# Kernel tuning notes

Measured on AMD Instinct MI355X. Metric: run time of the kernel, lower is better.

Reference implementation:

```python
import jax, jax.numpy as jnp
import numpy as np

C = 256
NUM_HEADS = 4
GROUPS = 8
EPS = 1e-5


def setup_inputs() -> dict:
    key = jax.random.key(0)
    ks = jax.random.split(key, 7)
    B, H, W = 4, 64, 64
    x = jax.random.normal(ks[0], (B, C, H, W), dtype=jnp.float32)
    # GroupNorm affine params
    norm_w = jnp.ones((C,), dtype=jnp.float32)
    norm_b = jnp.zeros((C,), dtype=jnp.float32)
    # 1x1 convs == channel-mixing matrices
    qkv_w = jax.random.normal(ks[1], (3 * C, C), dtype=jnp.float32) * (C ** -0.5)
    qkv_b = jnp.zeros((3 * C,), dtype=jnp.float32)
    proj_w = jax.random.normal(ks[2], (C, C), dtype=jnp.float32) * (C ** -0.5)
    proj_b = jnp.zeros((C,), dtype=jnp.float32)
    return {"x": x, "norm_w": norm_w, "norm_b": norm_b,
            "qkv_w": qkv_w, "qkv_b": qkv_b,
            "proj_w": proj_w, "proj_b": proj_b}


def _group_norm(x, w, b):
    B, Cc, H, W = x.shape
    xr = x.reshape(B, GROUPS, Cc // GROUPS, H * W)
    mean = xr.mean(axis=(2, 3), keepdims=True)
    var = xr.var(axis=(2, 3), keepdims=True)
    xn = ((xr - mean) * jax.lax.rsqrt(var + EPS)).reshape(B, Cc, H, W)
    return xn * w[None, :, None, None] + b[None, :, None, None]


def reference(x, norm_w, norm_b, qkv_w, qkv_b, proj_w, proj_b):
    B, Cc, H, W = x.shape
    nh = NUM_HEADS
    d = Cc // nh
    h = _group_norm(x, norm_w, norm_b)
    # 1x1 conv: channel matmul
    qkv = jnp.einsum('oc,bchw->bohw', qkv_w, h) + qkv_b[None, :, None, None]
    q, k, v = jnp.split(qkv, 3, axis=1)
    q = q.reshape(B, nh, d, H * W)
    k = k.reshape(B, nh, d, H * W)
    v = v.reshape(B, nh, d, H * W)
    scale = d ** -0.5
    attn = jnp.einsum('bhci,bhcj->bhij', q, k) * scale  # [B, nh, HW, HW]
    attn = jax.nn.softmax(attn, axis=-1)
    o = jnp.einsum('bhij,bhcj->bhci', attn, v).reshape(B, Cc, H, W)
    out = jnp.einsum('oc,bchw->bohw', proj_w, o) + proj_b[None, :, None, None]
    return x + out
```

## Files before the change

kernel.cpp:

```cpp
#include <hip/hip_runtime.h>

typedef unsigned short u16;
typedef __attribute__((ext_vector_type(8))) short bf16x8;
typedef __attribute__((ext_vector_type(4))) float f32x4;
typedef __attribute__((ext_vector_type(16))) float f32x16;
typedef __attribute__((ext_vector_type(2))) int i32x2;

#define MFMA16(A, B, C) __builtin_amdgcn_mfma_f32_16x16x32_bf16((A), (B), (C), 0, 0, 0)
#define MFMA32(A, B, C) __builtin_amdgcn_mfma_f32_32x32x16_bf16((A), (B), (C), 0, 0, 0)

#define BB 4
#define CC 256
#define HW 4096
#define NH 4
#define HD 64

#define QSCALE 0.18033688f

__device__ __forceinline__ u16 f2bf(float f) {
  unsigned int u = __builtin_bit_cast(unsigned int, f);
  u += 0x7fffu + ((u >> 16) & 1u);
  return (u16)(u >> 16);
}

__device__ __forceinline__ unsigned cvtpk(float a, float b) {
  unsigned r;
  asm("v_cvt_pk_bf16_f32 %0, %1, %2" : "=v"(r) : "v"(a), "v"(b));
  return r;
}

__global__ __launch_bounds__(256) void w2bf_kernel(const float* __restrict__ qw,
                                                   const float* __restrict__ pw,
                                                   u16* __restrict__ wbf) {
  int idx = (blockIdx.x * 256 + threadIdx.x) * 4;
  const int NQ = 768 * 256;
  const float* src = (idx < NQ) ? (qw + idx) : (pw + (idx - NQ));
  float4 v = *(const float4*)src;
  union { u16 u[4]; uint2 w; } pk;
  pk.u[0] = f2bf(v.x); pk.u[1] = f2bf(v.y);
  pk.u[2] = f2bf(v.z); pk.u[3] = f2bf(v.w);
  *(uint2*)(wbf + idx) = pk.w;
}

__global__ __launch_bounds__(256) void gn_partial_kernel(const float* __restrict__ x,
                                                         float* __restrict__ partial) {
  const float4* p = (const float4*)(x + (size_t)blockIdx.x * 16384);
  float s = 0.f, ss = 0.f;
  for (int i = threadIdx.x; i < 4096; i += 256) {
    float4 v = p[i];
    s += (v.x + v.y) + (v.z + v.w);
    ss += (v.x * v.x + v.y * v.y) + (v.z * v.z + v.w * v.w);
  }
#pragma unroll
  for (int msk = 32; msk; msk >>= 1) {
    s += __shfl_xor(s, msk);
    ss += __shfl_xor(ss, msk);
  }
  __shared__ float red[2][4];
  int wave = threadIdx.x >> 6;
  if ((threadIdx.x & 63) == 0) { red[0][wave] = s; red[1][wave] = ss; }
  __syncthreads();
  if (threadIdx.x == 0) {
    partial[blockIdx.x] = red[0][0] + red[0][1] + red[0][2] + red[0][3];
    partial[256 + blockIdx.x] = red[1][0] + red[1][1] + red[1][2] + red[1][3];
  }
}

__global__ __launch_bounds__(64) void gn_final_kernel(const float* __restrict__ partial,
                                                      float* __restrict__ stats) {
  int bg = threadIdx.x;
  if (bg < 32) {
    float S = 0.f, SS = 0.f;
#pragma unroll
    for (int sp = 0; sp < 8; ++sp) {
      S += partial[bg * 8 + sp];
      SS += partial[256 + bg * 8 + sp];
    }
    const float invN = 1.0f / 131072.0f;
    float mean = S * invN;
    float var = SS * invN - mean * mean;
    stats[bg] = mean;
    stats[32 + bg] = rsqrtf(var + 1e-5f);
  }
}

__global__ __launch_bounds__(256) void norm_t_kernel(const float* __restrict__ x,
                                                     const float* __restrict__ nw,
                                                     const float* __restrict__ nb,
                                                     const float* __restrict__ stats,
                                                     u16* __restrict__ h_t) {
  int b = blockIdx.y;
  int s = blockIdx.x * 64 + (threadIdx.x & 63);
  int w = threadIdx.x >> 6;
  const float* xb = x + (size_t)b * CC * HW;
  u16* hb = h_t + ((size_t)b * HW + s) * CC;
#pragma unroll
  for (int cc = 0; cc < 8; ++cc) {
    int c0 = w * 64 + cc * 8;
    union { u16 u[8]; uint4 v; } pk;
#pragma unroll
    for (int j = 0; j < 8; ++j) {
      int c = c0 + j;
      int g = c >> 5;
      float mean = stats[b * 8 + g];
      float rstd = stats[32 + b * 8 + g];
      float a = nw[c] * rstd;
      float bb2 = nb[c] - mean * a;
      float vv = xb[(size_t)c * HW + s];
      pk.u[j] = f2bf(vv * a + bb2);
    }
    *(uint4*)(hb + c0) = pk.v;
  }
}

__global__ __launch_bounds__(256) void gemm_qk_kernel(const u16* __restrict__ h_t,
                                                      const u16* __restrict__ wbf,
                                                      const float* __restrict__ qb,
                                                      u16* __restrict__ q_t,
                                                      u16* __restrict__ k_t) {
  int b = blockIdx.z;
  int lane = threadIdx.x & 63, wave = threadIdx.x >> 6;
  int lr = lane & 15, lg = lane >> 4;
  int m0 = blockIdx.x * 128 + (wave >> 1) * 64;
  int n0 = blockIdx.y * 128 + (wave & 1) * 64;
  const u16* hb = h_t + (size_t)b * HW * CC;
  f32x4 acc[4][4] = {};
  for (int kc = 0; kc < 8; ++kc) {
    int ko = kc * 32 + lg * 8;
    bf16x8 af[4], bfr[4];
#pragma unroll
    for (int mi = 0; mi < 4; ++mi)
      af[mi] = *(const bf16x8*)(hb + (size_t)(m0 + mi * 16 + lr) * CC + ko);
#pragma unroll
    for (int ni = 0; ni < 4; ++ni)
      bfr[ni] = *(const bf16x8*)(wbf + (size_t)(n0 + ni * 16 + lr) * CC + ko);
#pragma unroll
    for (int mi = 0; mi < 4; ++mi)
#pragma unroll
      for (int ni = 0; ni < 4; ++ni)
        acc[mi][ni] = MFMA16(af[mi], bfr[ni], acc[mi][ni]);
  }
  bool isq = (blockIdx.y < 2);
  u16* dst = isq ? q_t : k_t;
  float scl = isq ? QSCALE : 1.0f;
#pragma unroll
  for (int ni = 0; ni < 4; ++ni) {
    int o = n0 + ni * 16 + lr;
    float bias = qb[o];
    int oc = isq ? o : (o - 256);
    u16* dp = dst + (((size_t)b * NH + (oc >> 6)) * HW) * HD + (oc & 63);
#pragma unroll
    for (int mi = 0; mi < 4; ++mi)
#pragma unroll
      for (int r = 0; r < 4; ++r) {
        int s = m0 + mi * 16 + lg * 4 + r;
        dp[(size_t)s * HD] = f2bf((acc[mi][ni][r] + bias) * scl);
      }
  }
}

__global__ __launch_bounds__(256) void gemm_v_kernel(const u16* __restrict__ h_t,
                                                     const u16* __restrict__ wbf,
                                                     const float* __restrict__ qb,
                                                     u16* __restrict__ v_o) {
  int b = blockIdx.z;
  int lane = threadIdx.x & 63, wave = threadIdx.x >> 6;
  int lr = lane & 15, lg = lane >> 4;
  int m0 = blockIdx.y * 128 + (wave >> 1) * 64;
  int n0 = blockIdx.x * 128 + (wave & 1) * 64;
  const u16* hb = h_t + (size_t)b * HW * CC;
  f32x4 acc[4][4] = {};
  for (int kc = 0; kc < 8; ++kc) {
    int ko = kc * 32 + lg * 8;
    bf16x8 af[4], bfr[4];
#pragma unroll
    for (int mi = 0; mi < 4; ++mi)
      af[mi] = *(const bf16x8*)(wbf + (size_t)(512 + m0 + mi * 16 + lr) * CC + ko);
#pragma unroll
    for (int ni = 0; ni < 4; ++ni)
      bfr[ni] = *(const bf16x8*)(hb + (size_t)(n0 + ni * 16 + lr) * CC + ko);
#pragma unroll
    for (int mi = 0; mi < 4; ++mi)
#pragma unroll
      for (int ni = 0; ni < 4; ++ni)
        acc[mi][ni] = MFMA16(af[mi], bfr[ni], acc[mi][ni]);
  }
#pragma unroll
  for (int mi = 0; mi < 4; ++mi)
#pragma unroll
    for (int r = 0; r < 4; ++r) {
      int o = m0 + mi * 16 + lg * 4 + r;
      float bias = qb[512 + o];
      u16* vp = v_o + (((size_t)b * NH + (o >> 6)) * HD + (o & 63)) * HW;
#pragma unroll
      for (int ni = 0; ni < 4; ++ni) {
        int s = n0 + ni * 16 + lr;
        vp[s] = f2bf(acc[mi][ni][r] + bias);
      }
    }
}

__global__ __launch_bounds__(256) void attn_kernel(const u16* __restrict__ q_t,
                                                   const u16* __restrict__ k_t,
                                                   const u16* __restrict__ v,
                                                   u16* __restrict__ o_t) {
  __shared__ __align__(16) short k_lds[2][4096];
  __shared__ __align__(16) short v_lds[2][4096];
  int bh = blockIdx.y;
  int tid = threadIdx.x;
  int wave = tid >> 6, lane = tid & 63;
  int ql = lane & 31, hi = lane >> 5;
  int q0w = blockIdx.x * 128 + wave * 32;
  const u16* qp = q_t + (size_t)bh * HW * HD;
  const u16* kp = k_t + (size_t)bh * HW * HD;
  const u16* vp = v + (size_t)bh * HD * HW;

  bf16x8 qf[4];
#pragma unroll
  for (int kc = 0; kc < 4; ++kc)
    qf[kc] = *(const bf16x8*)(qp + (size_t)(q0w + ql) * HD + kc * 16 + hi * 8);

  int xr = (ql & 7) << 4;
  int xoff[4];
#pragma unroll
  for (int kc = 0; kc < 4; ++kc) xoff[kc] = (kc * 32 + hi * 16) ^ xr;

  int krow = tid >> 3, kcol = (tid & 7) * 8;
  const u16* kg = kp + (size_t)krow * HD + kcol;
  const u16* vg = vp + (size_t)krow * HW + kcol;
  int swb0 = krow * 128 + ((kcol * 2) ^ ((krow & 7) << 4));
  int swb1 = swb0 + 32 * 128;

  float m_run = -1e30f, l_run = 0.f;
  f32x16 of0 = {}, of1 = {};
  bf16x8 pf[4];

  uint4 kr0, kr1, vr0, vr1, t0, t1;
  t0 = *(const uint4*)(kg);
  t1 = *(const uint4*)(kg + 32 * HD);
  kr0 = *(const uint4*)(kg + 64 * HD);
  kr1 = *(const uint4*)(kg + 96 * HD);
  vr0 = *(const uint4*)(vg);
  vr1 = *(const uint4*)(vg + 32 * HW);
  *(uint4*)((char*)k_lds[0] + swb0) = t0;
  *(uint4*)((char*)k_lds[0] + swb1) = t1;
  asm volatile("s_waitcnt lgkmcnt(0)" ::: "memory");
  __builtin_amdgcn_s_barrier();

  for (int it = 0; it < 64; ++it) {
    int cur = it & 1;
    *(uint4*)((char*)v_lds[cur] + swb0) = vr0;
    *(uint4*)((char*)v_lds[cur] + swb1) = vr1;
    if (it < 63) {
      *(uint4*)((char*)k_lds[cur ^ 1] + swb0) = kr0;
      *(uint4*)((char*)k_lds[cur ^ 1] + swb1) = kr1;
    }
    if (it < 62) {
      int jb = (it + 2) * 64;
      kr0 = *(const uint4*)(kg + (size_t)jb * HD);
      kr1 = *(const uint4*)(kg + (size_t)(jb + 32) * HD);
    }
    if (it < 63) {
      int jb = (it + 1) * 64;
      vr0 = *(const uint4*)(vg + jb);
      vr1 = *(const uint4*)(vg + 32 * HW + jb);
    }
    const char* kb_base = (const char*)k_lds[cur];
    const char* vb_base = (const char*)v_lds[cur ^ 1];

    f32x16 s0 = {}, s1 = {};
    __builtin_amdgcn_s_setprio(1);
#pragma unroll
    for (int kc = 0; kc < 4; ++kc) {
      bf16x8 a0 = *(const bf16x8*)(kb_base + ql * 128 + xoff[kc]);
      bf16x8 a1 = *(const bf16x8*)(kb_base + (32 + ql) * 128 + xoff[kc]);
      s0 = MFMA32(a0, qf[kc], s0);
      s1 = MFMA32(a1, qf[kc], s1);
    }
    if (it > 0) {
#pragma unroll
      for (int kc = 0; kc < 4; ++kc) {
        bf16x8 av0 = *(const bf16x8*)(vb_base + ql * 128 + xoff[kc]);
        bf16x8 av1 = *(const bf16x8*)(vb_base + (32 + ql) * 128 + xoff[kc]);
        of0 = MFMA32(av0, pf[kc], of0);
        of1 = MFMA32(av1, pf[kc], of1);
      }
    }
    __builtin_amdgcn_s_setprio(0);

    float m8[8];
#pragma unroll
    for (int i = 0; i < 8; ++i)
      m8[i] = fmaxf(fmaxf(s0[i], s0[i + 8]), fmaxf(s1[i], s1[i + 8]));
    float m4a = fmaxf(m8[0], m8[4]), m4b = fmaxf(m8[1], m8[5]);
    float m4c = fmaxf(m8[2], m8[6]), m4d = fmaxf(m8[3], m8[7]);
    float mx = fmaxf(fmaxf(m4a, m4b), fmaxf(m4c, m4d));
    mx = fmaxf(mx, __shfl_xor(mx, 32));

    if (!__all(mx <= m_run + 8.0f)) {
      float mn = fmaxf(m_run, mx);
      float alpha = __builtin_amdgcn_exp2f(m_run - mn);
      m_run = mn;
      l_run *= alpha;
      of0 *= alpha;
      of1 *= alpha;
    }
#pragma unroll
    for (int i = 0; i < 16; ++i) {
      s0[i] = __builtin_amdgcn_exp2f(s0[i] - m_run);
      s1[i] = __builtin_amdgcn_exp2f(s1[i] - m_run);
    }
    float t8[8];
#pragma unroll
    for (int i = 0; i < 8; ++i)
      t8[i] = (s0[i] + s0[i + 8]) + (s1[i] + s1[i + 8]);
    float t4a = t8[0] + t8[4], t4b = t8[1] + t8[5];
    float t4c = t8[2] + t8[6], t4d = t8[3] + t8[7];
    l_run += (t4a + t4b) + (t4c + t4d);

#pragma unroll
    for (int kc = 0; kc < 4; ++kc) {
      const f32x16 pv = (kc < 2) ? s0 : s1;
      const int b8 = (kc & 1) * 8;
      unsigned A0 = cvtpk(pv[b8 + 0], pv[b8 + 1]);
      unsigned A1 = cvtpk(pv[b8 + 2], pv[b8 + 3]);
      unsigned B0 = cvtpk(pv[b8 + 4], pv[b8 + 5]);
      unsigned B1 = cvtpk(pv[b8 + 6], pv[b8 + 7]);
      i32x2 r0 = __builtin_amdgcn_permlane32_swap((int)A0, (int)B0, false, false);
      i32x2 r1 = __builtin_amdgcn_permlane32_swap((int)A1, (int)B1, false, false);
      union { unsigned w[4]; bf16x8 v8; } u;
      u.w[0] = (unsigned)r0[0]; u.w[1] = (unsigned)r1[0];
      u.w[2] = (unsigned)r0[1]; u.w[3] = (unsigned)r1[1];
      pf[kc] = u.v8;
    }

    asm volatile("s_waitcnt lgkmcnt(0)" ::: "memory");
    __builtin_amdgcn_s_barrier();
  }

  {
    const char* vb_base = (const char*)v_lds[1];
    __builtin_amdgcn_s_setprio(1);
#pragma unroll
    for (int kc = 0; kc < 4; ++kc) {
      bf16x8 av0 = *(const bf16x8*)(vb_base + ql * 128 + xoff[kc]);
      bf16x8 av1 = *(const bf16x8*)(vb_base + (32 + ql) * 128 + xoff[kc]);
      of0 = MFMA32(av0, pf[kc], of0);
      of1 = MFMA32(av1, pf[kc], of1);
    }
    __builtin_amdgcn_s_setprio(0);
  }

  float l_tot = l_run + __shfl_xor(l_run, 32);
  float inv_l = 1.0f / l_tot;
  int bb = bh >> 2, hh = bh & 3;
  u16* orow = o_t + ((size_t)bb * HW + q0w + ql) * CC + hh * 64;
#pragma unroll
  for (int cb = 0; cb < 2; ++cb) {
    const f32x16 o = cb ? of1 : of0;
#pragma unroll
    for (int t = 0; t < 4; ++t) {
      int c0 = cb * 32 + t * 8 + hi * 4;
      union { u16 u[4]; uint2 w; } pk;
#pragma unroll
      for (int r = 0; r < 4; ++r) pk.u[r] = f2bf(o[t * 4 + r] * inv_l);
      *(uint2*)(orow + c0) = pk.w;
    }
  }
}

__global__ __launch_bounds__(256) void proj_kernel(const u16* __restrict__ o_t,
                                                   const u16* __restrict__ wbf,
                                                   const float* __restrict__ pb,
                                                   const float* __restrict__ x,
                                                   float* __restrict__ out) {
  int b = blockIdx.z;
  int lane = threadIdx.x & 63, wave = threadIdx.x >> 6;
  int lr = lane & 15, lg = lane >> 4;
  int m0 = blockIdx.x * 128 + (wave >> 1) * 64;
  int n0 = blockIdx.y * 128 + (wave & 1) * 64;
  const u16* ob = o_t + (size_t)b * HW * CC;
  const u16* pwbf = wbf + (size_t)768 * CC;
  f32x4 acc[4][4] = {};
  for (int kc = 0; kc < 8; ++kc) {
    int ko = kc * 32 + lg * 8;
    bf16x8 af[4], bfr[4];
#pragma unroll
    for (int mi = 0; mi < 4; ++mi)
      af[mi] = *(const bf16x8*)(ob + (size_t)(m0 + mi * 16 + lr) * CC + ko);
#pragma unroll
    for (int ni = 0; ni < 4; ++ni)
      bfr[ni] = *(const bf16x8*)(pwbf + (size_t)(n0 + ni * 16 + lr) * CC + ko);
#pragma unroll
    for (int mi = 0; mi < 4; ++mi)
#pragma unroll
      for (int ni = 0; ni < 4; ++ni)
        acc[mi][ni] = MFMA16(af[mi], bfr[ni], acc[mi][ni]);
  }
#pragma unroll
  for (int ni = 0; ni < 4; ++ni) {
    int o = n0 + ni * 16 + lr;
    float bias = pb[o];
    const float* xp = x + ((size_t)b * CC + o) * HW;
    float* op = out + ((size_t)b * CC + o) * HW;
#pragma unroll
    for (int mi = 0; mi < 4; ++mi) {
      int sb = m0 + mi * 16 + lg * 4;
      float4 xv = *(const float4*)(xp + sb);
      float4 res;
      res.x = acc[mi][ni][0] + bias + xv.x;
      res.y = acc[mi][ni][1] + bias + xv.y;
      res.z = acc[mi][ni][2] + bias + xv.z;
      res.w = acc[mi][ni][3] + bias + xv.w;
      *(float4*)(op + sb) = res;
    }
  }
}

extern "C" void kernel_launch(void* const* d_in, const int* in_sizes, int n_in,
                              void* d_out, int out_size, void* d_ws, size_t ws_size,
                              hipStream_t stream) {
  const float* x = (const float*)d_in[0];
  const float* nw = (const float*)d_in[1];
  const float* nb = (const float*)d_in[2];
  const float* qw = (const float*)d_in[3];
  const float* qb = (const float*)d_in[4];
  const float* pw = (const float*)d_in[5];
  const float* pb = (const float*)d_in[6];
  float* out = (float*)d_out;

  float* stats = (float*)d_ws;
  float* partial = stats + 64;
  u16* h_t = (u16*)((char*)d_ws + 4096);
  u16* q_t = h_t + (size_t)BB * HW * CC;
  u16* k_t = q_t + (size_t)BB * HW * CC;
  u16* v_b = k_t + (size_t)BB * HW * CC;
  u16* wbf = v_b + (size_t)BB * HW * CC;
  u16* o_t = h_t;

  gn_partial_kernel<<<256, 256, 0, stream>>>(x, partial);
  gn_final_kernel<<<1, 64, 0, stream>>>(partial, stats);
  w2bf_kernel<<<256, 256, 0, stream>>>(qw, pw, wbf);
  norm_t_kernel<<<dim3(HW / 64, BB), 256, 0, stream>>>(x, nw, nb, stats, h_t);
  gemm_qk_kernel<<<dim3(HW / 128, 4, BB), 256, 0, stream>>>(h_t, wbf, qb, q_t, k_t);
  gemm_v_kernel<<<dim3(HW / 128, 2, BB), 256, 0, stream>>>(h_t, wbf, qb, v_b);
  attn_kernel<<<dim3(HW / 128, BB * NH), 256, 0, stream>>>(q_t, k_t, v_b, o_t);
  proj_kernel<<<dim3(HW / 128, 2, BB), 256, 0, stream>>>(o_t, wbf, pb, x, out);
}
```

Baseline: 164.4 us.

## Load K/V fragments directly from global into registers, dropping LDS staging

The attention kernel no longer stages K and V tiles through double-buffered shared memory with barriers. Each wave now loads its MFMA operand fragments straight from global memory into registers, prefetching the next K block, and does the PV product in the same iteration instead of one step behind. This removes the LDS writes, LDS reads and block barriers. In exchange, every wave of a block fetches the same K/V data separately, so global/L2 traffic rises about fourfold and more latency is exposed, since V is loaded in the same iteration it is used.

```diff
diff --git a/kernel.cpp b/kernel.cpp
--- a/kernel.cpp
+++ b/kernel.cpp
@@ -204,8 +204,6 @@
                                                    const u16* __restrict__ k_t,
                                                    const u16* __restrict__ v,
                                                    u16* __restrict__ o_t) {
-  __shared__ __align__(16) short k_lds[2][4096];
-  __shared__ __align__(16) short v_lds[2][4096];
   int bh = blockIdx.y;
   int tid = threadIdx.x;
   int wave = tid >> 6, lane = tid & 63;
@@ -220,73 +218,45 @@
   for (int kc = 0; kc < 4; ++kc)
     qf[kc] = *(const bf16x8*)(qp + (size_t)(q0w + ql) * HD + kc * 16 + hi * 8);
 
-  int xr = (ql & 7) << 4;
-  int xoff[4];
-#pragma unroll
-  for (int kc = 0; kc < 4; ++kc) xoff[kc] = (kc * 32 + hi * 16) ^ xr;
-
-  int krow = tid >> 3, kcol = (tid & 7) * 8;
-  const u16* kg = kp + (size_t)krow * HD + kcol;
-  const u16* vg = vp + (size_t)krow * HW + kcol;
-  int swb0 = krow * 128 + ((kcol * 2) ^ ((krow & 7) << 4));
-  int swb1 = swb0 + 32 * 128;
+  const u16* kgp = kp + (size_t)ql * HD + hi * 8;
+  const u16* vgp = vp + (size_t)ql * HW + hi * 8;
 
   float m_run = -1e30f, l_run = 0.f;
   f32x16 of0 = {}, of1 = {};
-  bf16x8 pf[4];
-
-  uint4 kr0, kr1, vr0, vr1, t0, t1;
-  t0 = *(const uint4*)(kg);
-  t1 = *(const uint4*)(kg + 32 * HD);
-  kr0 = *(const uint4*)(kg + 64 * HD);
-  kr1 = *(const uint4*)(kg + 96 * HD);
-  vr0 = *(const uint4*)(vg);
-  vr1 = *(const uint4*)(vg + 32 * HW);
-  *(uint4*)((char*)k_lds[0] + swb0) = t0;
-  *(uint4*)((char*)k_lds[0] + swb1) = t1;
-  asm volatile("s_waitcnt lgkmcnt(0)" ::: "memory");
-  __builtin_amdgcn_s_barrier();
-
+  bf16x8 kf[8], vf[8];
+
+#pragma unroll
+  for (int kc = 0; kc < 4; ++kc) {
+    kf[kc * 2 + 0] = *(const bf16x8*)(kgp + kc * 16);
+    kf[kc * 2 + 1] = *(const bf16x8*)(kgp + (size_t)32 * HD + kc * 16);
+  }
+
+#pragma unroll 1
   for (int it = 0; it < 64; ++it) {
-    int cur = it & 1;
-    *(uint4*)((char*)v_lds[cur] + swb0) = vr0;
-    *(uint4*)((char*)v_lds[cur] + swb1) = vr1;
-    if (it < 63) {
-      *(uint4*)((char*)k_lds[cur ^ 1] + swb0) = kr0;
-      *(uint4*)((char*)k_lds[cur ^ 1] + swb1) = kr1;
-    }
-    if (it < 62) {
-      int jb = (it + 2) * 64;
-      kr0 = *(const uint4*)(kg + (size_t)jb * HD);
-      kr1 = *(const uint4*)(kg + (size_t)(jb + 32) * HD);
-    }
-    if (it < 63) {
-      int jb = (it + 1) * 64;
-      vr0 = *(const uint4*)(vg + jb);
-      vr1 = *(const uint4*)(vg + 32 * HW + jb);
-    }
-    const char* kb_base = (const char*)k_lds[cur];
-    const char* vb_base = (const char*)v_lds[cur ^ 1];
+    int jb = it * 64;
+#pragma unroll
+    for (int kc = 0; kc < 4; ++kc) {
+      vf[kc * 2 + 0] = *(const bf16x8*)(vgp + jb + kc * 16);
+      vf[kc * 2 + 1] = *(const bf16x8*)(vgp + (size_t)32 * HW + jb + kc * 16);
+    }
 
     f32x16 s0 = {}, s1 = {};
     __builtin_amdgcn_s_setprio(1);
 #pragma unroll
     for (int kc = 0; kc < 4; ++kc) {
-      bf16x8 a0 = *(const bf16x8*)(kb_base + ql * 128 + xoff[kc]);
-      bf16x8 a1 = *(const bf16x8*)(kb_base + (32 + ql) * 128 + xoff[kc]);
-      s0 = MFMA32(a0, qf[kc], s0);
-      s1 = MFMA32(a1, qf[kc], s1);
-    }
-    if (it > 0) {
+      s0 = MFMA32(kf[kc * 2 + 0], qf[kc], s0);
+      s1 = MFMA32(kf[kc * 2 + 1], qf[kc], s1);
+    }
+    __builtin_amdgcn_s_setprio(0);
+
+    if (it < 63) {
+      const u16* kn = kgp + (size_t)(jb + 64) * HD;
 #pragma unroll
       for (int kc = 0; kc < 4; ++kc) {
-        bf16x8 av0 = *(const bf16x8*)(vb_base + ql * 128 + xoff[kc]);
-        bf16x8 av1 = *(const bf16x8*)(vb_base + (32 + ql) * 128 + xoff[kc]);
-        of0 = MFMA32(av0, pf[kc], of0);
-        of1 = MFMA32(av1, pf[kc], of1);
+        kf[kc * 2 + 0] = *(const bf16x8*)(kn + kc * 16);
+        kf[kc * 2 + 1] = *(const bf16x8*)(kn + (size_t)32 * HD + kc * 16);
       }
     }
-    __builtin_amdgcn_s_setprio(0);
 
     float m8[8];
 #pragma unroll
@@ -318,6 +288,7 @@
     float t4c = t8[2] + t8[6], t4d = t8[3] + t8[7];
     l_run += (t4a + t4b) + (t4c + t4d);
 
+    bf16x8 pf[4];
 #pragma unroll
     for (int kc = 0; kc < 4; ++kc) {
       const f32x16 pv = (kc < 2) ? s0 : s1;
@@ -334,19 +305,11 @@
       pf[kc] = u.v8;
     }
 
-    asm volatile("s_waitcnt lgkmcnt(0)" ::: "memory");
-    __builtin_amdgcn_s_barrier();
-  }
-
-  {
-    const char* vb_base = (const char*)v_lds[1];
     __builtin_amdgcn_s_setprio(1);
 #pragma unroll
     for (int kc = 0; kc < 4; ++kc) {
-      bf16x8 av0 = *(const bf16x8*)(vb_base + ql * 128 + xoff[kc]);
-      bf16x8 av1 = *(const bf16x8*)(vb_base + (32 + ql) * 128 + xoff[kc]);
-      of0 = MFMA32(av0, pf[kc], of0);
-      of1 = MFMA32(av1, pf[kc], of1);
+      of0 = MFMA32(vf[kc * 2 + 0], pf[kc], of0);
+      of1 = MFMA32(vf[kc * 2 + 1], pf[kc], of1);
     }
     __builtin_amdgcn_s_setprio(0);
   }
```

Measured after the change: 296.8 us. 1.81x slower.
